# Kernel optimization log

Measured on AMD Instinct MI355X. Metric: run time of the kernel, lower is better.

## Reference

```python
import jax, jax.numpy as jnp
import numpy as np

B, H, V, DEPTH = 64, 1024, 32000, 5


def setup_inputs() -> dict:
    key = jax.random.key(0)
    ks = jax.random.split(key, 9)
    s = 1.0 / np.sqrt(H)
    u = lambda k, shape: jax.random.uniform(k, shape, jnp.float32, -s, s)
    return {
        "encoding": jax.random.normal(ks[0], (B, H), jnp.float32),
        "Whh_l": u(ks[1], (3 * H, H)),
        "bih_l": u(ks[2], (3 * H,)),
        "bhh_l": u(ks[3], (3 * H,)),
        "Whh_r": u(ks[4], (3 * H, H)),
        "bih_r": u(ks[5], (3 * H,)),
        "bhh_r": u(ks[6], (3 * H,)),
        "W_out": u(ks[7], (V, H)),
        "b_out": u(ks[8], (V,)),
        "depth": DEPTH,
    }


def _gru_zero_input(h, Whh, bih, bhh):
    # PyTorch GRU cell with x == 0: W_ih @ x vanishes, only b_ih survives.
    d = h.shape[-1]
    gh = h @ Whh.T + bhh                                   # [N, 3H]
    r = jax.nn.sigmoid(bih[:d] + gh[..., :d])
    z = jax.nn.sigmoid(bih[d:2 * d] + gh[..., d:2 * d])
    n = jnp.tanh(bih[2 * d:] + r * gh[..., 2 * d:])
    return (1.0 - z) * n + z * h


def reference(encoding, Whh_l, bih_l, bhh_l, Whh_r, bih_r, bhh_r, W_out, b_out, depth):
    b, h = encoding.shape
    cur = encoding[:, None, :]                             # [B, 1, H] roots
    for _ in range(depth):                                 # expand perfect binary tree, level-batched
        n = cur.shape[1]
        flat = cur.reshape(b * n, h)
        left = _gru_zero_input(flat, Whh_l, bih_l, bhh_l).reshape(b, n, h)
        right = _gru_zero_input(flat, Whh_r, bih_r, bhh_r).reshape(b, n, h)
        cur = jnp.stack([left, right], axis=2).reshape(b, 2 * n, h)  # interleave children
    logits = jnp.einsum("blh,vh->blv", cur, W_out) + b_out  # [B, L, V]
    return jax.nn.log_softmax(logits, axis=-1)
```

## Files before the change

### kernel.cpp

```cpp
#include <hip/hip_runtime.h>
#include <hip/hip_bf16.h>
#include <cstdint>
#include <cstddef>

#define H_DIM   1024
#define B_DIM   64
#define V_DIM   32000
#define DEPTH_C 5

using bf16x8  = __attribute__((ext_vector_type(8))) __bf16;
using bf16x4  = __attribute__((ext_vector_type(4))) __bf16;
using floatx4 = __attribute__((ext_vector_type(4))) float;

__device__ __forceinline__ void gl_lds16(const __bf16* g, __bf16* l) {
  __builtin_amdgcn_global_load_lds(
      (const __attribute__((address_space(1))) unsigned int*)g,
      (__attribute__((address_space(3))) unsigned int*)l, 16, 0, 0);
}

__global__ __launch_bounds__(256) void f2b(const float* __restrict__ in,
                                           __bf16* __restrict__ out, int n) {
  for (int i = (blockIdx.x * 256 + threadIdx.x) * 4; i < n;
       i += gridDim.x * 1024) {
    float4 v = *(const float4*)(in + i);
    bf16x4 o;
    o[0] = (__bf16)v.x; o[1] = (__bf16)v.y; o[2] = (__bf16)v.z; o[3] = (__bf16)v.w;
    *(bf16x4*)(out + i) = o;
  }
}

__device__ __forceinline__ bf16x8 cvt8(float4 a, float4 b) {
  bf16x8 r;
  r[0] = (__bf16)a.x; r[1] = (__bf16)a.y; r[2] = (__bf16)a.z; r[3] = (__bf16)a.w;
  r[4] = (__bf16)b.x; r[5] = (__bf16)b.y; r[6] = (__bf16)b.z; r[7] = (__bf16)b.w;
  return r;
}

#define VMCNT(n) asm volatile("s_waitcnt vmcnt(" #n ")" ::: "memory")
#define LGK0()                                  \
  do {                                          \
    asm volatile("s_waitcnt lgkmcnt(0)" ::: "memory"); \
    __builtin_amdgcn_sched_barrier(0);          \
  } while (0)
#define SBAR()                                  \
  do {                                          \
    __builtin_amdgcn_sched_barrier(0);          \
    __builtin_amdgcn_s_barrier();               \
    __builtin_amdgcn_sched_barrier(0);          \
  } while (0)
#define LDA(MH, KS)                                                          \
  do {                                                                       \
    _Pragma("unroll") for (int mf = 0; mf < 4; ++mf)                         \
        aF[mf] = *(const bf16x8*)(cb + aRow + (MH)*8192 + mf * 2048 +        \
                                  ((KS) ? cksw1 : cksw0));                   \
  } while (0)
#define LDB(KS)                                                              \
  do {                                                                       \
    _Pragma("unroll") for (int nj = 0; nj < 4; ++nj)                         \
        bB[nj] = *(const bf16x8*)(cb + 32768 + bRow + nj * 2048 +            \
                                  ((KS) ? cksw1 : cksw0));                   \
  } while (0)
#define MM(MH)                                                               \
  do {                                                                       \
    __builtin_amdgcn_s_setprio(1);                                           \
    _Pragma("unroll") for (int mf = 0; mf < 4; ++mf)                         \
        _Pragma("unroll") for (int nj = 0; nj < 4; ++nj)                     \
            acc[(MH)*4 + mf][nj] = __builtin_amdgcn_mfma_f32_16x16x32_bf16(  \
                aF[mf], bB[nj], acc[(MH)*4 + mf][nj], 0, 0, 0);              \
    __builtin_amdgcn_s_setprio(0);                                           \
  } while (0)

__global__ __launch_bounds__(512, 2) void gemm_logits_8ph(
    const __bf16* __restrict__ A, const __bf16* __restrict__ Wb,
    float* __restrict__ Cf, const float* __restrict__ bias,
    float2* __restrict__ part) {
  __shared__ __align__(16) char smem[131072];

  const int tid = threadIdx.x;
  int h = blockIdx.y * 8 + blockIdx.x;
  h = (h & 7) * 125 + (h >> 3);
  const int bx = h & 7, by = h >> 3;
  const int m0 = bx * 256, n0 = by * 256;

  const int lane = tid & 63, wave = tid >> 6;
  const int wr = wave >> 2, wc = wave & 3;
  const int lrow = lane & 15, quad = lane >> 4;

  const int aRow  = (wr * 128 + lrow) * 128;
  const int bRow  = (wc * 64 + lrow) * 128;
  const int lsw   = (lrow & 7) << 4;
  const int cksw0 = (quad * 16) ^ lsw;
  const int cksw1 = (64 + quad * 16) ^ lsw;

  const int t8  = tid >> 3;
  const int cix = (tid & 7) ^ (t8 & 7);
  const __bf16* gA00 = A + (size_t)(m0 + t8) * 1024 + cix * 8;
  const __bf16* gA01 = A + (size_t)(m0 + 128 + t8) * 1024 + cix * 8;
  const __bf16* gA10 = gA00 + 64 * 1024;
  const __bf16* gA11 = gA01 + 64 * 1024;
  const __bf16* gB00 = Wb + (size_t)(n0 + t8) * 1024 + cix * 8;
  const __bf16* gB01 = Wb + (size_t)(n0 + 64 + t8) * 1024 + cix * 8;
  const __bf16* gB10 = gB00 + 128 * 1024;
  const __bf16* gB11 = gB01 + 128 * 1024;

  floatx4 acc[8][4] = {};
  bf16x8 aF[4], bB[4];

  gl_lds16(gA00, (__bf16*)(smem + tid * 16));
  gl_lds16(gA01, (__bf16*)(smem + 16384 + tid * 16));
  gl_lds16(gB00, (__bf16*)(smem + 32768 + tid * 16));
  gl_lds16(gB01, (__bf16*)(smem + 40960 + tid * 16));
  gl_lds16(gB10, (__bf16*)(smem + 49152 + tid * 16));
  gl_lds16(gB11, (__bf16*)(smem + 57344 + tid * 16));
  gl_lds16(gA10, (__bf16*)(smem + 8192 + tid * 16));
  gl_lds16(gA11, (__bf16*)(smem + 24576 + tid * 16));
  VMCNT(2);
  SBAR();

  for (int t = 0; t < 15; ++t) {
    char* cb = smem + (t & 1) * 65536;
    char* nb = smem + ((t & 1) ^ 1) * 65536;
    const int ke = (t + 1) * 64;
    LDB(0); LDA(0, 0);
    gl_lds16(gA00 + ke, (__bf16*)(nb + tid * 16));
    gl_lds16(gA01 + ke, (__bf16*)(nb + 16384 + tid * 16));
    SBAR(); LGK0();
    MM(0);
    VMCNT(2); SBAR();
    LDA(1, 0);
    gl_lds16(gB00 + ke, (__bf16*)(nb + 32768 + tid * 16));
    gl_lds16(gB01 + ke, (__bf16*)(nb + 40960 + tid * 16));
    SBAR(); LGK0();
    MM(1);
    SBAR();
    LDB(1); LDA(0, 1);
    gl_lds16(gB10 + ke, (__bf16*)(nb + 49152 + tid * 16));
    gl_lds16(gB11 + ke, (__bf16*)(nb + 57344 + tid * 16));
    SBAR(); LGK0();
    MM(0);
    SBAR();
    LDA(1, 1);
    gl_lds16(gA10 + ke, (__bf16*)(nb + 8192 + tid * 16));
    gl_lds16(gA11 + ke, (__bf16*)(nb + 24576 + tid * 16));
    SBAR(); LGK0();
    MM(1);
    VMCNT(2); SBAR();
  }
  {
    char* cb = smem + 65536;
    LDB(0); LDA(0, 0); MM(0);
    VMCNT(0); SBAR();
    LDA(1, 0); MM(1);
    LDB(1); LDA(0, 1); MM(0);
    LDA(1, 1); MM(1);
  }

  float bv[4];
#pragma unroll
  for (int nj = 0; nj < 4; ++nj) bv[nj] = bias[n0 + wc * 64 + nj * 16 + lrow];

  float* pm = (float*)smem;
  float* ps = (float*)(smem + 4096);

#pragma unroll
  for (int mi = 0; mi < 8; ++mi) {
    const int rowb = wr * 128 + mi * 16 + quad * 4;
#pragma unroll
    for (int r = 0; r < 4; ++r) {
      const float v0 = acc[mi][0][r] + bv[0];
      const float v1 = acc[mi][1][r] + bv[1];
      const float v2 = acc[mi][2][r] + bv[2];
      const float v3 = acc[mi][3][r] + bv[3];
      const size_t rb = (size_t)(m0 + rowb + r) * V_DIM + n0 + wc * 64 + lrow;
      Cf[rb]      = v0;
      Cf[rb + 16] = v1;
      Cf[rb + 32] = v2;
      Cf[rb + 48] = v3;
      float mx = fmaxf(fmaxf(v0, v1), fmaxf(v2, v3));
#pragma unroll
      for (int msk = 1; msk < 16; msk <<= 1)
        mx = fmaxf(mx, __shfl_xor(mx, msk, 64));
      float sm = __expf(v0 - mx) + __expf(v1 - mx) + __expf(v2 - mx) +
                 __expf(v3 - mx);
#pragma unroll
      for (int msk = 1; msk < 16; msk <<= 1) sm += __shfl_xor(sm, msk, 64);
      if (lrow == 0) {
        pm[(rowb + r) * 4 + wc] = mx;
        ps[(rowb + r) * 4 + wc] = sm;
      }
    }
  }
  __syncthreads();
  if (tid < 256) {
    float m = pm[tid * 4], s = ps[tid * 4];
#pragma unroll
    for (int w = 1; w < 4; ++w) {
      const float om = pm[tid * 4 + w], os = ps[tid * 4 + w];
      const float nm = fmaxf(m, om);
      s = s * __expf(m - nm) + os * __expf(om - nm);
      m = nm;
    }
    part[(size_t)(m0 + tid) * gridDim.y + by] = make_float2(m, s);
  }
}

__global__ __launch_bounds__(256) void gemm_tree(
    const __bf16* __restrict__ A, const __bf16* __restrict__ Wb0,
    const __bf16* __restrict__ Wb1, __bf16* __restrict__ Cb, int M) {
  constexpr int K = H_DIM;
  __shared__ __align__(16) __bf16 As[2][128 * 32];
  __shared__ __align__(16) __bf16 Bs[2][64 * 32];

  const int tid = threadIdx.x;
  const int nbx = gridDim.x;
  const int nwg = nbx * gridDim.y;
  int hflat = blockIdx.y * nbx + blockIdx.x;
  if ((nwg & 7) == 0) {
    const int cpx = nwg >> 3;
    hflat = (hflat & 7) * cpx + (hflat >> 3);
  }
  const int bx = hflat % nbx;
  const int by = hflat / nbx;
  const int m0 = bx * 128;
  const int n0 = by * 64;
  const int lane = tid & 63, wave = tid >> 6;
  const int lrow = lane & 15, quad = lane >> 4;
  const int wm = wave * 32;

  const __bf16* Wb = Wb0;
  int nw0 = n0;
  if (n0 >= 3072) { Wb = Wb1; nw0 = n0 - 3072; }

  const int sr = tid >> 2;
  const int sk = (tid & 3) * 8;
  int ra0 = m0 + sr;      if (ra0 >= M) ra0 = M - 1;
  int ra1 = m0 + sr + 64; if (ra1 >= M) ra1 = M - 1;
  const __bf16* ga0 = A + (size_t)ra0 * K + sk;
  const __bf16* ga1 = A + (size_t)ra1 * K + sk;
  const __bf16* gb0 = Wb + (size_t)(nw0 + sr) * K + sk;

  floatx4 acc[2][4] = {};

  gl_lds16(ga0, As[0] + tid * 8);
  gl_lds16(ga1, As[0] + 2048 + tid * 8);
  gl_lds16(gb0, Bs[0] + tid * 8);
  VMCNT(0);
  __syncthreads();

  int cur = 0;
  for (int kt = 0; kt < K; kt += 32) {
    if (kt + 32 < K) {
      gl_lds16(ga0 + kt + 32, As[cur ^ 1] + tid * 8);
      gl_lds16(ga1 + kt + 32, As[cur ^ 1] + 2048 + tid * 8);
      gl_lds16(gb0 + kt + 32, Bs[cur ^ 1] + tid * 8);
    }
    bf16x8 af[2], bfr[4];
#pragma unroll
    for (int i = 0; i < 2; i++)
      af[i] = *(const bf16x8*)(&As[cur][(wm + i * 16 + lrow) * 32 + quad * 8]);
#pragma unroll
    for (int j = 0; j < 4; j++)
      bfr[j] = *(const bf16x8*)(&Bs[cur][(j * 16 + lrow) * 32 + quad * 8]);
#pragma unroll
    for (int i = 0; i < 2; i++)
#pragma unroll
      for (int j = 0; j < 4; j++)
        acc[i][j] = __builtin_amdgcn_mfma_f32_16x16x32_bf16(af[i], bfr[j],
                                                            acc[i][j], 0, 0, 0);
    if (kt + 32 < K) {
      VMCNT(0);
      __syncthreads();
      cur ^= 1;
    }
  }

#pragma unroll
  for (int i = 0; i < 2; i++) {
#pragma unroll
    for (int j = 0; j < 4; j++) {
      const int col = n0 + j * 16 + lrow;
#pragma unroll
      for (int r = 0; r < 4; r++) {
        const int row = m0 + wm + i * 16 + quad * 4 + r;
        if (row < M) Cb[(size_t)row * 6144 + col] = (__bf16)acc[i][j][r];
      }
    }
  }
}

template <int TN, bool LOGITS, bool WBF16>
__global__ __launch_bounds__(256) void gemm_nt(
    const __bf16* __restrict__ A, const __bf16* __restrict__ Wb0,
    const __bf16* __restrict__ Wb1, const float* __restrict__ Wf,
    __bf16* __restrict__ Cb, float* __restrict__ Cf,
    const float* __restrict__ bias, float2* __restrict__ part, int M, int N) {
  constexpr int K = H_DIM;
  constexpr int MI = (TN == 128) ? 4 : 2;
  __shared__ __align__(16) __bf16 As[128 * 32];
  __shared__ __align__(16) __bf16 Bs[TN * 32];

  const int tid  = threadIdx.x;
  const int nbx = gridDim.x;
  const int nwg = nbx * gridDim.y;
  int hflat = blockIdx.y * nbx + blockIdx.x;
  if ((nwg & 7) == 0) {
    const int cpx = nwg >> 3;
    hflat = (hflat & 7) * cpx + (hflat >> 3);
  }
  const int bx = hflat % nbx;
  const int by = hflat / nbx;
  const int m0   = bx * 128;
  const int n0   = by * TN;
  const int lane = tid & 63;
  const int wave = tid >> 6;
  const int lrow = lane & 15;
  const int quad = lane >> 4;
  const int wm   = (TN == 128) ? (wave >> 1) * 64 : wave * 32;
  const int wn   = (TN == 128) ? (wave & 1) * 64 : 0;

  const __bf16* Wb = Wb0;
  int nw0 = n0;
  if (!LOGITS && n0 >= 3072) { Wb = Wb1; nw0 = n0 - 3072; }

  const int sr = tid >> 2;
  const int sk = (tid & 3) * 8;

  int ra0 = m0 + sr;      if (ra0 >= M) ra0 = M - 1;
  int ra1 = m0 + sr + 64; if (ra1 >= M) ra1 = M - 1;
  const __bf16* ga0 = A + (size_t)ra0 * K + sk;
  const __bf16* ga1 = A + (size_t)ra1 * K + sk;
  const __bf16* gb0 = nullptr; const __bf16* gb1 = nullptr;
  const float* gf0 = nullptr; const float* gf1 = nullptr;
  if (WBF16) {
    gb0 = Wb + (size_t)(nw0 + sr) * K + sk;
    if (TN == 128) gb1 = Wb + (size_t)(nw0 + sr + 64) * K + sk;
  } else {
    gf0 = Wf + (size_t)(n0 + sr) * K + sk;
    gf1 = Wf + (size_t)(n0 + sr + 64) * K + sk;
  }

  floatx4 acc[MI][4] = {};

  for (int kt = 0; kt < K; kt += 32) {
    float4 w00, w01, w10, w11;
    if (!WBF16) {
      w00 = *(const float4*)(gf0 + kt);
      w01 = *(const float4*)(gf0 + kt + 4);
      w10 = *(const float4*)(gf1 + kt);
      w11 = *(const float4*)(gf1 + kt + 4);
    }
    __syncthreads();
    gl_lds16(ga0 + kt, As + tid * 8);
    gl_lds16(ga1 + kt, As + 2048 + tid * 8);
    if (WBF16) {
      gl_lds16(gb0 + kt, Bs + tid * 8);
      if (TN == 128) gl_lds16(gb1 + kt, Bs + 2048 + tid * 8);
    } else {
      *(bf16x8*)(&Bs[sr * 32 + sk])        = cvt8(w00, w01);
      *(bf16x8*)(&Bs[(sr + 64) * 32 + sk]) = cvt8(w10, w11);
    }
    __syncthreads();

    bf16x8 af[MI], bfr[4];
#pragma unroll
    for (int i = 0; i < MI; i++)
      af[i] = *(const bf16x8*)(&As[(wm + i * 16 + lrow) * 32 + quad * 8]);
#pragma unroll
    for (int j = 0; j < 4; j++)
      bfr[j] = *(const bf16x8*)(&Bs[(wn + j * 16 + lrow) * 32 + quad * 8]);
#pragma unroll
    for (int i = 0; i < MI; i++)
#pragma unroll
      for (int j = 0; j < 4; j++)
        acc[i][j] =
            __builtin_amdgcn_mfma_f32_16x16x32_bf16(af[i], bfr[j], acc[i][j], 0, 0, 0);
  }

  float bv[4];
  if constexpr (LOGITS) {
#pragma unroll
    for (int j = 0; j < 4; j++) bv[j] = bias[n0 + wn + j * 16 + lrow];
  }
#pragma unroll
  for (int i = 0; i < MI; i++) {
#pragma unroll
    for (int j = 0; j < 4; j++) {
      const int col = n0 + wn + j * 16 + lrow;
#pragma unroll
      for (int r = 0; r < 4; r++) {
        const int row = m0 + wm + i * 16 + quad * 4 + r;
        if (row < M) {
          if (LOGITS) Cf[(size_t)row * N + col] = acc[i][j][r] + bv[j];
          else        Cb[(size_t)row * N + col] = (__bf16)acc[i][j][r];
        }
      }
    }
  }

  if constexpr (LOGITS) {
    __shared__ float pmax[2][128], psum[2][128];
    const int wnh = wn >> 6;
#pragma unroll
    for (int i = 0; i < MI; i++) {
#pragma unroll
      for (int r = 0; r < 4; r++) {
        float mx = -3.0e38f;
#pragma unroll
        for (int j = 0; j < 4; j++) mx = fmaxf(mx, acc[i][j][r] + bv[j]);
#pragma unroll
        for (int mask = 1; mask < 16; mask <<= 1)
          mx = fmaxf(mx, __shfl_xor(mx, mask, 64));
        float sm = 0.f;
#pragma unroll
        for (int j = 0; j < 4; j++) sm += __expf(acc[i][j][r] + bv[j] - mx);
#pragma unroll
        for (int mask = 1; mask < 16; mask <<= 1)
          sm += __shfl_xor(sm, mask, 64);
        if (lrow == 0) {
          pmax[wnh][wm + i * 16 + quad * 4 + r] = mx;
          psum[wnh][wm + i * 16 + quad * 4 + r] = sm;
        }
      }
    }
    __syncthreads();
    if (tid < 128) {
      const float ma = pmax[0][tid], mb = pmax[1][tid];
      const float nm = fmaxf(ma, mb);
      const float ns = psum[0][tid] * __expf(ma - nm) +
                       psum[1][tid] * __expf(mb - nm);
      part[(size_t)(m0 + tid) * gridDim.y + by] = make_float2(nm, ns);
    }
  }
}

__global__ __launch_bounds__(256) void gru_gate(
    const __bf16* __restrict__ gh, const float* __restrict__ bih_l,
    const float* __restrict__ bhh_l, const float* __restrict__ bih_r,
    const float* __restrict__ bhh_r, const __bf16* __restrict__ hin,
    __bf16* __restrict__ hout, int n) {
  const int row = blockIdx.x;
  const int c = threadIdx.x * 4;
  const int b = row / n, j = row - b * n;
  const size_t g6 = (size_t)row * 6144;
  const bf16x4 h4 = *(const bf16x4*)(hin + (size_t)row * H_DIM + c);
  const size_t obase = (size_t)(b * 2 * n + 2 * j) * H_DIM;

  bf16x4 og[2];
#pragma unroll
  for (int side = 0; side < 2; ++side) {
    const float* bih = side ? bih_r : bih_l;
    const float* bhh = side ? bhh_r : bhh_l;
    const size_t gb = g6 + side * 3072;
    const bf16x4 g0 = *(const bf16x4*)(gh + gb + c);
    const bf16x4 g1 = *(const bf16x4*)(gh + gb + 1024 + c);
    const bf16x4 g2 = *(const bf16x4*)(gh + gb + 2048 + c);
    const float4 br0 = *(const float4*)(bih + c);
    const float4 br1 = *(const float4*)(bih + 1024 + c);
    const float4 br2 = *(const float4*)(bih + 2048 + c);
    const float4 bh0 = *(const float4*)(bhh + c);
    const float4 bh1 = *(const float4*)(bhh + 1024 + c);
    const float4 bh2 = *(const float4*)(bhh + 2048 + c);
    const float* pr0 = (const float*)&br0; const float* ph0 = (const float*)&bh0;
    const float* pr1 = (const float*)&br1; const float* ph1 = (const float*)&bh1;
    const float* pr2 = (const float*)&br2; const float* ph2 = (const float*)&bh2;
    bf16x4 o;
#pragma unroll
    for (int e = 0; e < 4; ++e) {
      const float gr = (float)g0[e] + ph0[e];
      const float gz = (float)g1[e] + ph1[e];
      const float gn = (float)g2[e] + ph2[e];
      const float r = 1.f / (1.f + __expf(-(pr0[e] + gr)));
      const float z = 1.f / (1.f + __expf(-(pr1[e] + gz)));
      const float nn = tanhf(pr2[e] + r * gn);
      o[e] = (__bf16)((1.f - z) * nn + z * (float)h4[e]);
    }
    og[side] = o;
  }
  *(bf16x4*)(hout + obase + c) = og[0];
  *(bf16x4*)(hout + obase + H_DIM + c) = og[1];
}

__global__ __launch_bounds__(256) void lsm_finish(
    float* __restrict__ out, const float2* __restrict__ part, int nb) {
  const int row = blockIdx.x;
  const int tid = threadIdx.x;

  float m = -3.0e38f, s = 0.f;
  if (tid < nb) {
    const float2 p = part[(size_t)row * nb + tid];
    m = p.x; s = p.y;
  }
#pragma unroll
  for (int off = 32; off; off >>= 1) {
    float om = __shfl_xor(m, off, 64);
    float os = __shfl_xor(s, off, 64);
    float nm = fmaxf(m, om);
    s = s * __expf(m - nm) + os * __expf(om - nm);
    m = nm;
  }
  __shared__ float rm[4], rs[4];
  if ((tid & 63) == 0) { rm[tid >> 6] = m; rs[tid >> 6] = s; }
  __syncthreads();
  const float M4 = fmaxf(fmaxf(rm[0], rm[1]), fmaxf(rm[2], rm[3]));
  const float S4 = rs[0] * __expf(rm[0] - M4) + rs[1] * __expf(rm[1] - M4) +
                   rs[2] * __expf(rm[2] - M4) + rs[3] * __expf(rm[3] - M4);
  const float lg = M4 + __logf(S4);

  float4* p4 = (float4*)(out + (size_t)row * V_DIM);
  for (int i = tid; i < 8000; i += 256) {
    float4 v = p4[i];
    v.x -= lg; v.y -= lg; v.z -= lg; v.w -= lg;
    p4[i] = v;
  }
}

extern "C" void kernel_launch(void* const* d_in, const int* in_sizes, int n_in,
                              void* d_out, int out_size, void* d_ws,
                              size_t ws_size, hipStream_t stream) {
  const float* enc   = (const float*)d_in[0];
  const float* Whh_l = (const float*)d_in[1];
  const float* bih_l = (const float*)d_in[2];
  const float* bhh_l = (const float*)d_in[3];
  const float* Whh_r = (const float*)d_in[4];
  const float* bih_r = (const float*)d_in[5];
  const float* bhh_r = (const float*)d_in[6];
  const float* W_out = (const float*)d_in[7];
  const float* b_out = (const float*)d_in[8];
  float* out = (float*)d_out;

  char* ws = (char*)d_ws;
  __bf16* ghb    = (__bf16*)ws;
  __bf16* buf0   = (__bf16*)(ws + 12582912);
  __bf16* buf1   = (__bf16*)(ws + 16777216);
  __bf16* WhhB_l = (__bf16*)(ws + 20971520);
  __bf16* WhhB_r = WhhB_l + 3145728;
  __bf16* encB   = (__bf16*)(ws + 33554432);
  __bf16* WoutB  = (__bf16*)(ws + 33685504);
  float2* part   = (float2*)ghb;
  const bool big = ws_size >= (size_t)(33685504 + 65536000);

  f2b<<<256, 256, 0, stream>>>(Whh_l, WhhB_l, 3 * H_DIM * H_DIM);
  f2b<<<256, 256, 0, stream>>>(Whh_r, WhhB_r, 3 * H_DIM * H_DIM);
  f2b<<<64, 256, 0, stream>>>(enc, encB, B_DIM * H_DIM);
  if (big) f2b<<<1024, 256, 0, stream>>>(W_out, WoutB, V_DIM * H_DIM);

  const __bf16* cur = encB;
  __bf16* nxt = buf0;
  int n = 1;
  for (int d = 0; d < DEPTH_C; d++) {
    const int M = B_DIM * n;
    dim3 gg((M + 127) / 128, 6144 / 64);
    gemm_tree<<<gg, 256, 0, stream>>>(cur, WhhB_l, WhhB_r, ghb, M);
    gru_gate<<<dim3(M), 256, 0, stream>>>(ghb, bih_l, bhh_l, bih_r, bhh_r,
                                          cur, nxt, n);
    cur = nxt;
    nxt = (nxt == buf0) ? buf1 : buf0;
    n *= 2;
  }

  if (big) {
    gemm_logits_8ph<<<dim3(8, 125), 512, 0, stream>>>(cur, WoutB, out, b_out,
                                                      part);
    lsm_finish<<<2048, 256, 0, stream>>>(out, part, 125);
  } else {
    dim3 gf(2048 / 128, V_DIM / 128);
    gemm_nt<128, true, false><<<gf, 256, 0, stream>>>(
        cur, nullptr, nullptr, W_out, nullptr, out, b_out, part, 2048, V_DIM);
    lsm_finish<<<2048, 256, 0, stream>>>(out, part, 250);
  }
}
```

Measured before the change: 736.1 us.

## Stage logits epilogue through swizzled LDS and triple-buffer tree GEMM loads

The logits GEMM epilogue now writes bias-added accumulators into an XOR-swizzled LDS tile, half a block at a time. It then reads full rows back so each wave stores coalesced float4 rows of the fp32 logits and computes the row max and sum-exp with one wave-wide reduction. This replaces strided scalar stores and the cross-wave partial merge. Separately, the tree GRU GEMM moves from double to triple buffering with a vmcnt-based wait so global-to-LDS loads run two tiles ahead, at the cost of more LDS and extra barriers in the epilogue.

```diff
diff --git a/kernel.cpp b/kernel.cpp
--- a/kernel.cpp
+++ b/kernel.cpp
@@ -159,48 +159,47 @@
 #pragma unroll
   for (int nj = 0; nj < 4; ++nj) bv[nj] = bias[n0 + wc * 64 + nj * 16 + lrow];
 
-  float* pm = (float*)smem;
-  float* ps = (float*)(smem + 4096);
-
-#pragma unroll
-  for (int mi = 0; mi < 8; ++mi) {
-    const int rowb = wr * 128 + mi * 16 + quad * 4;
-#pragma unroll
-    for (int r = 0; r < 4; ++r) {
-      const float v0 = acc[mi][0][r] + bv[0];
-      const float v1 = acc[mi][1][r] + bv[1];
-      const float v2 = acc[mi][2][r] + bv[2];
-      const float v3 = acc[mi][3][r] + bv[3];
-      const size_t rb = (size_t)(m0 + rowb + r) * V_DIM + n0 + wc * 64 + lrow;
-      Cf[rb]      = v0;
-      Cf[rb + 16] = v1;
-      Cf[rb + 32] = v2;
-      Cf[rb + 48] = v3;
-      float mx = fmaxf(fmaxf(v0, v1), fmaxf(v2, v3));
-#pragma unroll
-      for (int msk = 1; msk < 16; msk <<= 1)
-        mx = fmaxf(mx, __shfl_xor(mx, msk, 64));
-      float sm = __expf(v0 - mx) + __expf(v1 - mx) + __expf(v2 - mx) +
-                 __expf(v3 - mx);
-#pragma unroll
-      for (int msk = 1; msk < 16; msk <<= 1) sm += __shfl_xor(sm, msk, 64);
-      if (lrow == 0) {
-        pm[(rowb + r) * 4 + wc] = mx;
-        ps[(rowb + r) * 4 + wc] = sm;
+  float* lf = (float*)smem;
+
+  __syncthreads();
+#pragma unroll
+  for (int half = 0; half < 2; ++half) {
+    if (half) __syncthreads();
+    if (wr == half) {
+#pragma unroll
+      for (int mi = 0; mi < 8; ++mi) {
+#pragma unroll
+        for (int nj = 0; nj < 4; ++nj) {
+          const int colg = wc * 16 + nj * 4 + (lrow >> 2);
+          const int cole = lrow & 3;
+#pragma unroll
+          for (int r = 0; r < 4; ++r) {
+            const int rowL = mi * 16 + quad * 4 + r;
+            lf[rowL * 256 + ((colg ^ (rowL & 7)) << 2) + cole] =
+                acc[mi][nj][r] + bv[nj];
+          }
+        }
       }
     }
-  }
-  __syncthreads();
-  if (tid < 256) {
-    float m = pm[tid * 4], s = ps[tid * 4];
-#pragma unroll
-    for (int w = 1; w < 4; ++w) {
-      const float om = pm[tid * 4 + w], os = ps[tid * 4 + w];
-      const float nm = fmaxf(m, om);
-      s = s * __expf(m - nm) + os * __expf(om - nm);
-      m = nm;
-    }
-    part[(size_t)(m0 + tid) * gridDim.y + by] = make_float2(m, s);
+    __syncthreads();
+#pragma unroll
+    for (int it = 0; it < 16; ++it) {
+      const int rowL = it * 8 + wave;
+      const int rsw  = rowL & 7;
+      const float4 v =
+          *(const float4*)&lf[rowL * 256 + ((lane ^ rsw) << 2)];
+      const int grow = m0 + half * 128 + rowL;
+      *(float4*)(Cf + (size_t)grow * V_DIM + n0 + lane * 4) = v;
+      float mx = fmaxf(fmaxf(v.x, v.y), fmaxf(v.z, v.w));
+#pragma unroll
+      for (int off = 32; off; off >>= 1) mx = fmaxf(mx, __shfl_xor(mx, off, 64));
+      float sm = __expf(v.x - mx) + __expf(v.y - mx) + __expf(v.z - mx) +
+                 __expf(v.w - mx);
+#pragma unroll
+      for (int off = 32; off; off >>= 1) sm += __shfl_xor(sm, off, 64);
+      if (lane == 0)
+        part[(size_t)grow * gridDim.y + by] = make_float2(mx, sm);
+    }
   }
 }
 
@@ -208,8 +207,8 @@
     const __bf16* __restrict__ A, const __bf16* __restrict__ Wb0,
     const __bf16* __restrict__ Wb1, __bf16* __restrict__ Cb, int M) {
   constexpr int K = H_DIM;
-  __shared__ __align__(16) __bf16 As[2][128 * 32];
-  __shared__ __align__(16) __bf16 Bs[2][64 * 32];
+  __shared__ __align__(16) __bf16 As[3][128 * 32];
+  __shared__ __align__(16) __bf16 Bs[3][64 * 32];
 
   const int tid = threadIdx.x;
   const int nbx = gridDim.x;
@@ -241,38 +240,39 @@
 
   floatx4 acc[2][4] = {};
 
-  gl_lds16(ga0, As[0] + tid * 8);
-  gl_lds16(ga1, As[0] + 2048 + tid * 8);
-  gl_lds16(gb0, Bs[0] + tid * 8);
+#define TSTAGE(T, BUF)                                     \
+  do {                                                     \
+    gl_lds16(ga0 + (T) * 32, As[BUF] + tid * 8);           \
+    gl_lds16(ga1 + (T) * 32, As[BUF] + 2048 + tid * 8);    \
+    gl_lds16(gb0 + (T) * 32, Bs[BUF] + tid * 8);           \
+  } while (0)
+#define TCOMP(CB)                                                            \
+  do {                                                                       \
+    bf16x8 af[2], bfr[4];                                                    \
+    _Pragma("unroll") for (int i = 0; i < 2; i++)                            \
+        af[i] = *(const bf16x8*)(&As[CB][(wm + i * 16 + lrow) * 32 +         \
+                                         quad * 8]);                         \
+    _Pragma("unroll") for (int j = 0; j < 4; j++)                            \
+        bfr[j] = *(const bf16x8*)(&Bs[CB][(j * 16 + lrow) * 32 + quad * 8]); \
+    _Pragma("unroll") for (int i = 0; i < 2; i++)                            \
+        _Pragma("unroll") for (int j = 0; j < 4; j++)                        \
+            acc[i][j] = __builtin_amdgcn_mfma_f32_16x16x32_bf16(             \
+                af[i], bfr[j], acc[i][j], 0, 0, 0);                          \
+  } while (0)
+
+  TSTAGE(0, 0);
+  TSTAGE(1, 1);
+  for (int t = 0; t < 31; ++t) {
+    VMCNT(3);
+    SBAR();
+    if (t + 2 < 32) TSTAGE(t + 2, (t + 2) % 3);
+    TCOMP(t % 3);
+  }
   VMCNT(0);
-  __syncthreads();
-
-  int cur = 0;
-  for (int kt = 0; kt < K; kt += 32) {
-    if (kt + 32 < K) {
-      gl_lds16(ga0 + kt + 32, As[cur ^ 1] + tid * 8);
-      gl_lds16(ga1 + kt + 32, As[cur ^ 1] + 2048 + tid * 8);
-      gl_lds16(gb0 + kt + 32, Bs[cur ^ 1] + tid * 8);
-    }
-    bf16x8 af[2], bfr[4];
-#pragma unroll
-    for (int i = 0; i < 2; i++)
-      af[i] = *(const bf16x8*)(&As[cur][(wm + i * 16 + lrow) * 32 + quad * 8]);
-#pragma unroll
-    for (int j = 0; j < 4; j++)
-      bfr[j] = *(const bf16x8*)(&Bs[cur][(j * 16 + lrow) * 32 + quad * 8]);
-#pragma unroll
-    for (int i = 0; i < 2; i++)
-#pragma unroll
-      for (int j = 0; j < 4; j++)
-        acc[i][j] = __builtin_amdgcn_mfma_f32_16x16x32_bf16(af[i], bfr[j],
-                                                            acc[i][j], 0, 0, 0);
-    if (kt + 32 < K) {
-      VMCNT(0);
-      __syncthreads();
-      cur ^= 1;
-    }
-  }
+  SBAR();
+  TCOMP(31 % 3);
+#undef TSTAGE
+#undef TCOMP
 
 #pragma unroll
   for (int i = 0; i < 2; i++) {
```

After: 749.0 us. About the same (+1.7%).
